# Optimization experiments

Measured on AMD Instinct MI355X. Metric: run time of the kernel, lower is better.

The kernel has to match this reference:

```python
import jax, jax.numpy as jnp
import numpy as np

N_NODES = 10000
N_EDGES = 320000
H = 8  # n_heads


def _heads(x, n_heads):
    # [E_or_N, m, 2d+1] -> [E_or_N, H, (m//H)*(2d+1)]  (fiber2head)
    n, m, c = x.shape
    return x.reshape(n, n_heads, (m // n_heads) * c)


def setup_inputs() -> dict:
    key = jax.random.key(0)
    ks = jax.random.split(key, 7)
    return {
        "v0": jax.random.normal(ks[0], (N_EDGES, 64, 1), dtype=jnp.float32),
        "v1": jax.random.normal(ks[1], (N_EDGES, 64, 3), dtype=jnp.float32),
        "k0": jax.random.normal(ks[2], (N_EDGES, 64, 1), dtype=jnp.float32),
        "k1": jax.random.normal(ks[3], (N_EDGES, 64, 3), dtype=jnp.float32),
        "q0": jax.random.normal(ks[4], (N_NODES, 64, 1), dtype=jnp.float32),
        "q1": jax.random.normal(ks[5], (N_NODES, 64, 3), dtype=jnp.float32),
        "dst": jax.random.randint(ks[6], (N_EDGES,), 0, N_NODES, dtype=jnp.int32),
    }


def reference(v0, v1, k0, k1, q0, q1, dst):
    # fiber2head: concat per-head-flattened features over degrees
    kh = jnp.concatenate([_heads(k0, H), _heads(k1, H)], axis=-1)  # [E,H,Dh]
    qh = jnp.concatenate([_heads(q0, H), _heads(q1, H)], axis=-1)  # [N,H,Dh]

    d_key = q0.shape[1] * q0.shape[2] + q1.shape[1] * q1.shape[2]  # f_key.n_features = 256

    # e_dot_v('k','q'): edge key . dst-node query, per head
    e = jnp.einsum('ehd,ehd->eh', kh, qh[dst]) / jnp.sqrt(jnp.float32(d_key))  # [E,H]

    # edge_softmax over incoming edges of each destination node
    emax = jax.ops.segment_max(e, dst, num_segments=N_NODES)  # [N,H]
    ex = jnp.exp(e - emax[dst])
    denom = jax.ops.segment_sum(ex, dst, num_segments=N_NODES)  # [N,H]
    a = ex / denom[dst]  # [E,H]

    def agg(v):
        E, m, c = v.shape
        vh = v.reshape(E, H, m // H, c)                      # [E,H,m/H,2d+1]
        msg = a[:, :, None, None] * vh                        # attn-weighted message
        out = jax.ops.segment_sum(msg, dst, num_segments=N_NODES)
        return out.reshape(N_NODES, m, c)                     # [N,m,2d+1]

    return agg(v0), agg(v1)
```

## Files before the change

kernel.cpp:

```cpp
#include <hip/hip_runtime.h>

#define NHEAD 8

__global__ __launch_bounds__(256) void edge_logits_kernel(
    const float* __restrict__ k0, const float* __restrict__ k1,
    const float* __restrict__ q0, const float* __restrict__ q1,
    const int* __restrict__ dst,
    float* __restrict__ exw,
    float* __restrict__ denom,
    int* __restrict__ cnt,
    int E)
{
    const int wid  = threadIdx.x >> 6;
    const int lane = threadIdx.x & 63;
    const int e = blockIdx.x * 4 + wid;
    if (e >= E) return;
    const int n = dst[e];

    const float kv0 = k0[e * 64 + lane];
    const float qv0 = q0[n * 64 + lane];
    const float3 kv1 = *(const float3*)(k1 + (size_t)e * 192 + lane * 3);
    const float3 qv1 = *(const float3*)(q1 + (size_t)n * 192 + lane * 3);

    float p = kv0 * qv0 + kv1.x * qv1.x + kv1.y * qv1.y + kv1.z * qv1.z;
    p += __shfl_xor(p, 1);
    p += __shfl_xor(p, 2);
    p += __shfl_xor(p, 4);

    if ((lane & 7) == 0) {
        const float ex = __expf(p * 0.0625f);
        const int h = lane >> 3;
        exw[e * NHEAD + h] = ex;
        atomicAdd(&denom[n * NHEAD + h], ex);
    }
    if (lane == 0) atomicAdd(&cnt[n], 1);
}

__global__ __launch_bounds__(1024) void scan_kernel(
    const int* __restrict__ cnt, int* __restrict__ offs,
    int* __restrict__ cursor, int n)
{
    __shared__ int sdata[1024];
    const int tid = threadIdx.x;
    const int items = (n + 1023) >> 10;
    const int base = tid * items;
    int local[16];
    int sum = 0;
    for (int i = 0; i < items && i < 16; ++i) {
        int idx = base + i;
        int v = (idx < n) ? cnt[idx] : 0;
        local[i] = sum;
        sum += v;
    }
    sdata[tid] = sum;
    __syncthreads();
    for (int off = 1; off < 1024; off <<= 1) {
        int v = (tid >= off) ? sdata[tid - off] : 0;
        __syncthreads();
        sdata[tid] += v;
        __syncthreads();
    }
    const int prev = (tid > 0) ? sdata[tid - 1] : 0;
    for (int i = 0; i < items && i < 16; ++i) {
        int idx = base + i;
        if (idx < n) {
            int o = prev + local[i];
            offs[idx] = o;
            cursor[idx] = o;
        }
    }
    if (tid == 0) offs[n] = sdata[1023];
}

__global__ __launch_bounds__(256) void scatter_kernel(
    const int* __restrict__ dst, int* __restrict__ cursor,
    int* __restrict__ eids, int E)
{
    const int e = blockIdx.x * 256 + threadIdx.x;
    if (e >= E) return;
    const int n = dst[e];
    const int p = atomicAdd(&cursor[n], 1);
    eids[p] = e;
}

__global__ __launch_bounds__(256) void agg_kernel(
    const float* __restrict__ v0, const float* __restrict__ v1,
    const float* __restrict__ exw, const float* __restrict__ denom,
    const int* __restrict__ offs, const int* __restrict__ eids,
    float* __restrict__ out, int N)
{
    __shared__ int se[256];
    const int n = blockIdx.x;
    const int t = threadIdx.x;
    const int h = (t < 64) ? (t >> 3) : ((t - 64) / 24);

    const int start = offs[n];
    const int end   = offs[n + 1];

    float acc = 0.f;
    for (int base = start; base < end; base += 256) {
        const int c = min(256, end - base);
        __syncthreads();
        if (t < c) se[t] = eids[base + t];
        __syncthreads();
        for (int i = 0; i < c; ++i) {
            const int e = se[i];
            const float w = exw[e * NHEAD + h];
            const float v = (t < 64) ? v0[e * 64 + t]
                                     : v1[(size_t)e * 192 + (t - 64)];
            acc += w * v;
        }
    }
    const float d = denom[n * NHEAD + h];
    const float invd = (end > start) ? (1.0f / d) : 0.0f;
    acc *= invd;

    if (t < 64) out[n * 64 + t] = acc;
    else        out[(size_t)N * 64 + (size_t)n * 192 + (t - 64)] = acc;
}

extern "C" void kernel_launch(void* const* d_in, const int* in_sizes, int n_in,
                              void* d_out, int out_size, void* d_ws, size_t ws_size,
                              hipStream_t stream) {
    const float* v0 = (const float*)d_in[0];
    const float* v1 = (const float*)d_in[1];
    const float* k0 = (const float*)d_in[2];
    const float* k1 = (const float*)d_in[3];
    const float* q0 = (const float*)d_in[4];
    const float* q1 = (const float*)d_in[5];
    const int*  dst = (const int*)d_in[6];

    const int E = in_sizes[6];
    const int N = in_sizes[4] / 64;

    char* ws = (char*)d_ws;
    size_t off = 0;
    float* exw = (float*)(ws + off);   off += (size_t)E * NHEAD * 4;
    float* denom = (float*)(ws + off); off += (size_t)N * NHEAD * 4;
    int* cnt = (int*)(ws + off);       off += (size_t)N * 4;
    size_t zero_from = (char*)denom - ws;
    size_t zero_len  = off - zero_from;
    int* offs = (int*)(ws + off);      off += (size_t)(N + 1) * 4;
    off = (off + 15) & ~(size_t)15;
    int* cursor = (int*)(ws + off);    off += (size_t)N * 4;
    off = (off + 15) & ~(size_t)15;
    int* eids = (int*)(ws + off);      off += (size_t)E * 4;

    hipMemsetAsync(ws + zero_from, 0, zero_len, stream);

    edge_logits_kernel<<<(E + 3) / 4, 256, 0, stream>>>(
        k0, k1, q0, q1, dst, exw, denom, cnt, E);

    scan_kernel<<<1, 1024, 0, stream>>>(cnt, offs, cursor, N);

    scatter_kernel<<<(E + 255) / 256, 256, 0, stream>>>(dst, cursor, eids, E);

    agg_kernel<<<N, 256, 0, stream>>>(
        v0, v1, exw, denom, offs, eids, (float*)d_out, N);
}
```

Measured before the change: 621.5 us.

## Fuse edge logit computation into per-node aggregation kernel

```diff
diff --git a/kernel.cpp b/kernel.cpp
--- a/kernel.cpp
+++ b/kernel.cpp
@@ -2,38 +2,11 @@
 
 #define NHEAD 8
 
-__global__ __launch_bounds__(256) void edge_logits_kernel(
-    const float* __restrict__ k0, const float* __restrict__ k1,
-    const float* __restrict__ q0, const float* __restrict__ q1,
-    const int* __restrict__ dst,
-    float* __restrict__ exw,
-    float* __restrict__ denom,
-    int* __restrict__ cnt,
-    int E)
+__global__ __launch_bounds__(256) void count_kernel(
+    const int* __restrict__ dst, int* __restrict__ cnt, int E)
 {
-    const int wid  = threadIdx.x >> 6;
-    const int lane = threadIdx.x & 63;
-    const int e = blockIdx.x * 4 + wid;
-    if (e >= E) return;
-    const int n = dst[e];
-
-    const float kv0 = k0[e * 64 + lane];
-    const float qv0 = q0[n * 64 + lane];
-    const float3 kv1 = *(const float3*)(k1 + (size_t)e * 192 + lane * 3);
-    const float3 qv1 = *(const float3*)(q1 + (size_t)n * 192 + lane * 3);
-
-    float p = kv0 * qv0 + kv1.x * qv1.x + kv1.y * qv1.y + kv1.z * qv1.z;
-    p += __shfl_xor(p, 1);
-    p += __shfl_xor(p, 2);
-    p += __shfl_xor(p, 4);
-
-    if ((lane & 7) == 0) {
-        const float ex = __expf(p * 0.0625f);
-        const int h = lane >> 3;
-        exw[e * NHEAD + h] = ex;
-        atomicAdd(&denom[n * NHEAD + h], ex);
-    }
-    if (lane == 0) atomicAdd(&cnt[n], 1);
+    const int e = blockIdx.x * 256 + threadIdx.x;
+    if (e < E) atomicAdd(&cnt[dst[e]], 1);
 }
 
 __global__ __launch_bounds__(1024) void scan_kernel(
@@ -83,40 +56,86 @@
     eids[p] = e;
 }
 
-__global__ __launch_bounds__(256) void agg_kernel(
+__global__ __launch_bounds__(256) void fused_kernel(
+    const float* __restrict__ k0, const float* __restrict__ k1,
+    const float* __restrict__ q0, const float* __restrict__ q1,
     const float* __restrict__ v0, const float* __restrict__ v1,
-    const float* __restrict__ exw, const float* __restrict__ denom,
     const int* __restrict__ offs, const int* __restrict__ eids,
     float* __restrict__ out, int N)
 {
-    __shared__ int se[256];
-    const int n = blockIdx.x;
-    const int t = threadIdx.x;
-    const int h = (t < 64) ? (t >> 3) : ((t - 64) / 24);
+    __shared__ int   se[256];
+    __shared__ float ex_s[2][8][NHEAD];
+    __shared__ float ds_s[4][NHEAD];
+
+    const int n    = blockIdx.x;
+    const int t    = threadIdx.x;
+    const int w    = t >> 6;
+    const int lane = t & 63;
 
     const int start = offs[n];
     const int end   = offs[n + 1];
 
-    float acc = 0.f;
-    for (int base = start; base < end; base += 256) {
-        const int c = min(256, end - base);
+    const float  qv0 = q0[(size_t)n * 64 + lane];
+    const float3 qv1 = *(const float3*)(q1 + (size_t)n * 192 + lane * 3);
+
+    const int j = t - 64;
+    const int h = (t < 64) ? (t >> 3) : (j / 24);
+    const float* vptr;
+    int vstride;
+    if (t < 64) { vptr = v0 + t; vstride = 64;  }
+    else        { vptr = v1 + j; vstride = 192; }
+
+    float acc  = 0.f;
+    float dsum = 0.f;
+    int buf = 0;
+
+    for (int cb = start; cb < end; cb += 256) {
+        const int c = min(256, end - cb);
         __syncthreads();
-        if (t < c) se[t] = eids[base + t];
+        if (t < c) se[t] = eids[cb + t];
         __syncthreads();
-        for (int i = 0; i < c; ++i) {
-            const int e = se[i];
-            const float w = exw[e * NHEAD + h];
-            const float v = (t < 64) ? v0[e * 64 + t]
-                                     : v1[(size_t)e * 192 + (t - 64)];
-            acc += w * v;
+
+        for (int g = 0; g < c; g += 8) {
+            #pragma unroll
+            for (int s = 0; s < 2; ++s) {
+                const int idx = g + w + s * 4;
+                float ex = 0.f;
+                if (idx < c) {
+                    const int e = se[idx];
+                    const float  kv0 = k0[(size_t)e * 64 + lane];
+                    const float3 kv1 = *(const float3*)(k1 + (size_t)e * 192 + lane * 3);
+                    float p = kv0 * qv0 + kv1.x * qv1.x + kv1.y * qv1.y
+                            + kv1.z * qv1.z;
+                    p += __shfl_xor(p, 1);
+                    p += __shfl_xor(p, 2);
+                    p += __shfl_xor(p, 4);
+                    ex = __expf(p * 0.0625f);
+                }
+                if ((lane & 7) == 0) ex_s[buf][w + s * 4][lane >> 3] = ex;
+                dsum += ex;
+            }
+            __syncthreads();
+
+            const int gc = min(8, c - g);
+            #pragma unroll
+            for (int jj = 0; jj < 8; ++jj) {
+                if (jj < gc) {
+                    const int e = se[g + jj];
+                    acc += ex_s[buf][jj][h] * vptr[(size_t)e * vstride];
+                }
+            }
+            buf ^= 1;
         }
     }
-    const float d = denom[n * NHEAD + h];
+
+    if ((lane & 7) == 0) ds_s[w][lane >> 3] = dsum;
+    __syncthreads();
+    const float d = ds_s[0][h] + ds_s[1][h] + ds_s[2][h] + ds_s[3][h];
     const float invd = (end > start) ? (1.0f / d) : 0.0f;
     acc *= invd;
 
-    if (t < 64) out[n * 64 + t] = acc;
-    else        out[(size_t)N * 64 + (size_t)n * 192 + (t - 64)] = acc;
+    if (t < 64) out[(size_t)n * 64 + t] = acc;
+    else        out[(size_t)N * 64 + (size_t)n * 192 + j] = acc;
 }
 
 extern "C" void kernel_launch(void* const* d_in, const int* in_sizes, int n_in,
@@ -135,26 +154,21 @@
 
     char* ws = (char*)d_ws;
     size_t off = 0;
-    float* exw = (float*)(ws + off);   off += (size_t)E * NHEAD * 4;
-    float* denom = (float*)(ws + off); off += (size_t)N * NHEAD * 4;
     int* cnt = (int*)(ws + off);       off += (size_t)N * 4;
-    size_t zero_from = (char*)denom - ws;
-    size_t zero_len  = off - zero_from;
     int* offs = (int*)(ws + off);      off += (size_t)(N + 1) * 4;
     off = (off + 15) & ~(size_t)15;
     int* cursor = (int*)(ws + off);    off += (size_t)N * 4;
     off = (off + 15) & ~(size_t)15;
     int* eids = (int*)(ws + off);      off += (size_t)E * 4;
 
-    hipMemsetAsync(ws + zero_from, 0, zero_len, stream);
+    hipMemsetAsync(cnt, 0, (size_t)N * 4, stream);
 
-    edge_logits_kernel<<<(E + 3) / 4, 256, 0, stream>>>(
-        k0, k1, q0, q1, dst, exw, denom, cnt, E);
+    count_kernel<<<(E + 255) / 256, 256, 0, stream>>>(dst, cnt, E);
 
     scan_kernel<<<1, 1024, 0, stream>>>(cnt, offs, cursor, N);
 
     scatter_kernel<<<(E + 255) / 256, 256, 0, stream>>>(dst, cursor, eids, E);
 
-    agg_kernel<<<N, 256, 0, stream>>>(
-        v0, v1, exw, denom, offs, eids, (float*)d_out, N);
+    fused_kernel<<<N, 256, 0, stream>>>(
+        k0, k1, q0, q1, v0, v1, offs, eids, (float*)d_out, N);
 }
```

New measurement: 672.7 us. 1.08x slower.
